# Optimization experiments

Hardware: AMD Instinct MI355X
Metric: run time of the kernel (lower is better)

Reference implementation:

```python
import math
import jax, jax.numpy as jnp
import numpy as np

MUL = 8      # multiplicity of 0e and 1o in irreps_in/out
KS = 5       # kernel spatial extent (diameter 5, steps 1 -> coords -2..2)
NB = 5       # num_radial_basis
RAD = 2.5    # diameter / 2


def _sus(t):
    # e3nn sus(x) = exp(-1/x) for x>0 else 0
    return jnp.where(t > 0.0, jnp.exp(-1.0 / jnp.where(t > 0.0, t, 1.0)), 0.0)


def _emb_sh():
    c = jnp.arange(-2.0, 3.0)
    lat = jnp.stack(jnp.meshgrid(c, c, c, indexing='ij'), axis=-1)  # (5,5,5,3)
    d = jnp.linalg.norm(lat, axis=-1)
    # soft_one_hot_linspace(basis='smooth_finite', cutoff=True)
    values = jnp.linspace(0.0, RAD, NB + 2)
    step = values[1] - values[0]
    diff = (d[..., None] - values[1:-1]) / step
    emb = 1.14136 * math.exp(2.0) * _sus(diff + 1.0) * _sus(1.0 - diff)  # (5,5,5,NB)
    # real spherical harmonics, lmax=2, normalize=True, normalization='component'
    safe = jnp.where(d > 0.0, d, 1.0)[..., None]
    u = jnp.where(d[..., None] > 0.0, lat / safe, 0.0)
    x, y, z = u[..., 0], u[..., 1], u[..., 2]
    s3, s5, s15 = math.sqrt(3.0), math.sqrt(5.0), math.sqrt(15.0)
    sh = jnp.stack([
        jnp.ones_like(x),
        s3 * x, s3 * y, s3 * z,
        s15 * x * z, s15 * x * y,
        s5 * (y * y - 0.5 * (x * x + z * z)),
        s15 * y * z, (s15 / 2.0) * (z * z - x * x),
    ], axis=-1)  # (5,5,5,9)
    return emb, sh


def _c121():
    # Clebsch-Gordan (w3j) for 1o x 2e -> 1o in the real e3nn basis, built from the
    # orthonormal symmetric-traceless matrix basis matching the l=2 SH component order.
    s2, s6 = math.sqrt(2.0), math.sqrt(6.0)
    S = np.zeros((5, 3, 3))
    S[0, 0, 2] = S[0, 2, 0] = 1.0 / s2            # xz
    S[1, 0, 1] = S[1, 1, 0] = 1.0 / s2            # xy
    S[2] = np.diag([-1.0, 2.0, -1.0]) / s6        # 2y^2 - x^2 - z^2
    S[3, 1, 2] = S[3, 2, 1] = 1.0 / s2            # yz
    S[4] = np.diag([-1.0, 0.0, 1.0]) / s2         # z^2 - x^2
    # w3j(1,2,1)[m,j,k] = S[j,m,k]/sqrt(5)  (fully symmetric since l1+l2+l3 even)
    return jnp.asarray(np.transpose(S, (1, 0, 2)) / math.sqrt(5.0), dtype=jnp.float32)


def _build_kernel(weight, emb, sh, c121, dtype):
    g = (KS, KS, KS)
    W = (emb @ weight) / float(KS * KS * KS)  # (5,5,5,320)
    w1, w2, w3, w4, w5 = [W[..., 64 * i:64 * (i + 1)].reshape(g + (MUL, MUL)) for i in range(5)]
    sh0, sh1, sh2 = sh[..., 0], sh[..., 1:4], sh[..., 4:9]
    pw0 = math.sqrt(1.0 / 16.0)   # output 0e: alpha=1, fan_in=8+8
    pw1 = math.sqrt(3.0 / 24.0)   # output 1o: alpha=3, fan_in=8+8+8
    inv_s3 = 1.0 / math.sqrt(3.0)
    K00 = pw0 * sh0[..., None, None] * w1                                   # (g,u,w)
    K01 = (pw1 * inv_s3) * jnp.einsum('xyzuw,xyzk->xyzuwk', w2, sh1)        # (g,u,w,k)
    K10 = (pw0 * inv_s3) * jnp.einsum('xyzuw,xyzm->xyzumw', w4, sh1)        # (g,u,m,w)
    T = jnp.einsum('xyzj,mjk->xyzmk', sh2, c121)                            # (g,m,k)
    eye3 = jnp.eye(3, dtype=dtype)
    K11 = pw1 * (inv_s3 * jnp.einsum('xyzuw,mk->xyzumwk', sh0[..., None, None] * w3, eye3)
                 + jnp.einsum('xyzuw,xyzmk->xyzumwk', w5, T))               # (g,u,m,w,k)
    D = 4 * MUL
    kern = jnp.zeros(g + (D, D), dtype=dtype)
    kern = kern.at[..., :MUL, :MUL].set(K00)
    kern = kern.at[..., :MUL, MUL:].set(K01.reshape(g + (MUL, 3 * MUL)))
    kern = kern.at[..., MUL:, :MUL].set(K10.reshape(g + (3 * MUL, MUL)))
    kern = kern.at[..., MUL:, MUL:].set(K11.reshape(g + (3 * MUL, 3 * MUL)))
    return jnp.transpose(kern, (4, 3, 0, 1, 2))  # 'xyzio->oixyz'


def reference(x, weight, w_sc0, w_sc1):
    emb, sh = _emb_sh()
    c121 = _c121()
    kern = _build_kernel(weight, emb, sh, c121, x.dtype)
    B, _, X, Y, Z = x.shape
    inv_s8 = 1.0 / math.sqrt(MUL)
    # self-connection: e3nn Linear, 0e->0e and 1o->1o blocks
    x0 = x[:, :MUL]
    x1 = x[:, MUL:].reshape(B, MUL, 3, X, Y, Z)
    sc0 = inv_s8 * jnp.einsum('uv,buxyz->bvxyz', w_sc0, x0)
    sc1 = inv_s8 * jnp.einsum('uv,bumxyz->bvmxyz', w_sc1, x1).reshape(B, 3 * MUL, X, Y, Z)
    sc = jnp.concatenate([sc0, sc1], axis=1)
    conv = jax.lax.conv_general_dilated(
        x, kern, window_strides=(1, 1, 1), padding=[(2, 2)] * 3,
        dimension_numbers=('NCDHW', 'OIDHW', 'NCDHW'))
    return sc + conv


def setup_inputs() -> dict:
    key = jax.random.key(0)
    k1, k2, k3, k4 = jax.random.split(key, 4)
    return {
        'x': jax.random.normal(k1, (2, 32, 64, 64, 64), dtype=jnp.float32),
        'weight': jax.random.normal(k2, (NB, 5 * MUL * MUL), dtype=jnp.float32),
        'w_sc0': jax.random.normal(k3, (MUL, MUL), dtype=jnp.float32),
        'w_sc1': jax.random.normal(k4, (MUL, MUL), dtype=jnp.float32),
    }
```

## Files before the change

kernel.cpp:

```cpp
#include <hip/hip_runtime.h>
#include <math.h>

typedef __attribute__((ext_vector_type(8))) short short8;
typedef __attribute__((ext_vector_type(4))) float f32x4;
typedef __attribute__((ext_vector_type(16))) float f32x16;

#define NTAP 125
#define DCH 32

static __device__ __forceinline__ unsigned short f2bf(float f) {
    union { float f; unsigned u; } v; v.f = f;
    unsigned u = v.u;
    return (unsigned short)((u + 0x7FFFu + ((u >> 16) & 1u)) >> 16);
}

static __device__ __forceinline__ void gld_lds16(const void* g, void* l) {
    __builtin_amdgcn_global_load_lds(
        (const __attribute__((address_space(1))) unsigned int*)g,
        (__attribute__((address_space(3))) unsigned int*)l, 16, 0, 0);
}

__global__ __launch_bounds__(128) void build_kern(
    const float* __restrict__ weight,
    const float* __restrict__ w_sc0,
    const float* __restrict__ w_sc1,
    float* __restrict__ kw)
{
    const int t = blockIdx.x;
    const int dx = t / 25, dy = (t / 5) % 5, dz = t % 5;
    const float px = dx - 2.0f, py = dy - 2.0f, pz = dz - 2.0f;
    const float d = sqrtf(px * px + py * py + pz * pz);

    const float stepv = 2.5f / 6.0f;
    const float embc = 1.14136f * expf(2.0f);
    float emb[5];
#pragma unroll
    for (int n = 0; n < 5; ++n) {
        float diff = (d - stepv * (float)(n + 1)) / stepv;
        float a = diff + 1.0f, bb = 1.0f - diff;
        float v = 0.0f;
        if (a > 0.0f && bb > 0.0f)
            v = embc * expf(-1.0f / a) * expf(-1.0f / bb);
        emb[n] = v;
    }

    const float inv_d = (d > 0.0f) ? 1.0f / d : 0.0f;
    const float ux = px * inv_d, uy = py * inv_d, uz = pz * inv_d;
    const float s3 = 1.73205081f, s5 = 2.23606798f, s15 = 3.87298335f;
    float sh[9];
    sh[0] = 1.0f;
    sh[1] = s3 * ux; sh[2] = s3 * uy; sh[3] = s3 * uz;
    sh[4] = s15 * ux * uz;
    sh[5] = s15 * ux * uy;
    sh[6] = s5 * (uy * uy - 0.5f * (ux * ux + uz * uz));
    sh[7] = s15 * uy * uz;
    sh[8] = 0.5f * s15 * (uz * uz - ux * ux);

    const float i_s2 = 0.70710678f, i_s6 = 0.40824829f, i_s5 = 0.44721360f;
    float T[3][3];
    T[0][0] = i_s5 * (-sh[6] * i_s6 - sh[8] * i_s2);
    T[0][1] = i_s5 * (sh[5] * i_s2);
    T[0][2] = i_s5 * (sh[4] * i_s2);
    T[1][0] = T[0][1];
    T[1][1] = i_s5 * (2.0f * sh[6] * i_s6);
    T[1][2] = i_s5 * (sh[7] * i_s2);
    T[2][0] = T[0][2];
    T[2][1] = T[1][2];
    T[2][2] = i_s5 * (-sh[6] * i_s6 + sh[8] * i_s2);

    __shared__ float Wt[320];
    for (int col = threadIdx.x; col < 320; col += 128) {
        float a = 0.0f;
#pragma unroll
        for (int n = 0; n < 5; ++n) a += emb[n] * weight[n * 320 + col];
        Wt[col] = a * (1.0f / 125.0f);
    }
    __syncthreads();

    const float pw0 = 0.25f;
    const float pw1 = 0.35355339f;
    const float inv_s3 = 0.57735027f;
    const float inv_s8 = 0.35355339f;

    for (int idx = threadIdx.x; idx < 1024; idx += 128) {
        const int o = idx >> 5, i = idx & 31;
        float val;
        if (o < 8) {
            if (i < 8) {
                val = pw0 * Wt[i * 8 + o];
            } else {
                const int u = (i - 8) / 3, m = (i - 8) % 3;
                val = pw0 * inv_s3 * Wt[192 + u * 8 + o] * sh[1 + m];
            }
        } else {
            const int v = (o - 8) / 3, k = (o - 8) % 3;
            if (i < 8) {
                val = pw1 * inv_s3 * Wt[64 + i * 8 + v] * sh[1 + k];
            } else {
                const int u = (i - 8) / 3, m = (i - 8) % 3;
                float tv = Wt[256 + u * 8 + v] * T[m][k];
                if (m == k) tv += inv_s3 * Wt[128 + u * 8 + v];
                val = pw1 * tv;
            }
        }
        if (t == 62) {
            if (o < 8 && i < 8) {
                val += inv_s8 * w_sc0[i * 8 + o];
            } else if (o >= 8 && i >= 8) {
                const int u = (i - 8) / 3, m = (i - 8) % 3;
                const int v = (o - 8) / 3, k = (o - 8) % 3;
                if (m == k) val += inv_s8 * w_sc1[u * 8 + v];
            }
        }
        kw[(i * NTAP + t) * DCH + o] = val;
    }
}

__global__ __launch_bounds__(128) void pack_b(
    const float* __restrict__ kw, unsigned short* __restrict__ kwb)
{
    const int t = blockIdx.x;
    const int tid = threadIdx.x;
    const int kh = tid >> 6, l = tid & 63;
    const int co = l & 31;
    const int cib = kh * 16 + (l >> 5) * 8;
    unsigned short v[8];
#pragma unroll
    for (int j = 0; j < 8; ++j)
        v[j] = f2bf(kw[((cib + j) * NTAP + t) * DCH + co]);
    uint4 o;
    o.x = (unsigned)v[0] | ((unsigned)v[1] << 16);
    o.y = (unsigned)v[2] | ((unsigned)v[3] << 16);
    o.z = (unsigned)v[4] | ((unsigned)v[5] << 16);
    o.w = (unsigned)v[6] | ((unsigned)v[7] << 16);
    *reinterpret_cast<uint4*>(kwb + ((size_t)(t * 2 + kh) * 64 + l) * 8) = o;
}

__global__ __launch_bounds__(256) void xpose(
    const float* __restrict__ x, unsigned short* __restrict__ xt)
{
    const int xx = blockIdx.x, yy = blockIdx.y, b = blockIdx.z;
    const int t = threadIdx.x;
    const int z = t & 63, part = t >> 6;
    const float* src = x + ((((size_t)b * 32) * 64 + xx) * 64 + yy) * 64 + z;
    unsigned short v[8];
#pragma unroll
    for (int j = 0; j < 8; ++j)
        v[j] = f2bf(src[(size_t)(part * 8 + j) * 262144]);
    uint4 o;
    o.x = (unsigned)v[0] | ((unsigned)v[1] << 16);
    o.y = (unsigned)v[2] | ((unsigned)v[3] << 16);
    o.z = (unsigned)v[4] | ((unsigned)v[5] << 16);
    o.w = (unsigned)v[6] | ((unsigned)v[7] << 16);
    *reinterpret_cast<uint4*>(
        xt + ((((size_t)b * 64 + xx) * 64 + yy) * 64 + z) * 32 + part * 8) = o;
}

__global__ void zero_fill(float4* p) {
    p[threadIdx.x] = make_float4(0.f, 0.f, 0.f, 0.f);
}

__global__ __launch_bounds__(512, 4) void conv_mfma(
    const unsigned short* __restrict__ xt,
    const unsigned short* __restrict__ kwb,
    const unsigned short* __restrict__ zpage,
    float* __restrict__ out)
{
    extern __shared__ unsigned short smem[];
    char* lds = (char*)smem;

    const int tid = threadIdx.x;
    const int lane = tid & 63;
    const int wv = tid >> 6;
    const int oy = wv >> 1, zh = wv & 1;
    const int x0 = blockIdx.x * 4, y0 = blockIdx.y * 4;
    const int b = blockIdx.z;
    const int l31 = lane & 31, hi = lane >> 5;

    int abase[5][2];
#pragma unroll
    for (int dz = 0; dz < 5; ++dz) {
        const int s = zh * 32 + l31 + dz;
#pragma unroll
        for (int kh = 0; kh < 2; ++kh) {
            const int cph = (kh * 2 + hi) ^ (s & 3);
            abase[dz][kh] = 51200 + ((((oy * 68 + s) << 2) | cph) << 4);
        }
    }
    const int bbase = lane * 16;

    int srow[3]; long long soff[3]; bool szok[3];
#pragma unroll
    for (int p = 0; p < 3; ++p) {
        const int c = tid + p * 512;
        const int row = c / 272;
        const int rem = c - row * 272;
        const int slot = rem >> 2;
        const int clog = (rem & 3) ^ (slot & 3);
        const int z = slot - 2;
        srow[p] = row;
        szok[p] = ((unsigned)z < 64u);
        soff[p] = (long long)row * 2048 + (long long)z * 32 + clog * 8;
    }

    int bsrc[7];
#pragma unroll
    for (int k = 0; k < 7; ++k) {
        const int c = tid + k * 512;
        const int tp = c >> 7, rem = c & 127;
        const int dxx = tp / 5, dzz = tp - dxx * 5;
        bsrc[k] = (dxx * 25 + dzz) * 128 + rem;
    }

    f32x16 acc[4];
#pragma unroll
    for (int ox = 0; ox < 4; ++ox)
#pragma unroll
        for (int e = 0; e < 16; ++e) acc[ox][e] = 0.0f;

    for (int dy = 0; dy < 5; ++dy) {
        const int yyb = y0 + dy - 2;
#pragma unroll
        for (int xl = 0; xl < 8; ++xl) {
            __syncthreads();
            if (xl == 0) {
#pragma unroll
                for (int k = 0; k < 7; ++k) {
                    const int c0 = wv * 64 + k * 512;
                    if (c0 < 3200) {
                        gld_lds16(kwb + ((size_t)(bsrc[k] + dy * 640)) * 8,
                                  lds + c0 * 16);
                    }
                }
            }
            {
                const int xx = x0 + xl - 2;
                const bool xok = ((unsigned)xx < 64u);
                const long long xyb =
                    (long long)(b * 64 + xx) * 131072 + (long long)yyb * 2048;
#pragma unroll
                for (int p = 0; p < 3; ++p) {
                    const int c0 = wv * 64 + p * 512;
                    if (c0 < 1088) {
                        const int yy = yyb + srow[p];
                        const bool ok =
                            xok && ((unsigned)yy < 64u) && szok[p];
                        const unsigned short* src =
                            ok ? (xt + xyb + soff[p]) : zpage;
                        gld_lds16(src, lds + 51200 + c0 * 16);
                    }
                }
            }
            __syncthreads();

#pragma unroll
            for (int dz = 0; dz < 5; ++dz) {
#pragma unroll
                for (int kh = 0; kh < 2; ++kh) {
                    const short8 a =
                        *reinterpret_cast<const short8*>(lds + abase[dz][kh]);
#pragma unroll
                    for (int ox = 0; ox < 4; ++ox) {
                        const int dxv = xl - ox;
                        if (dxv < 0 || dxv > 4) continue;
                        const short8 bf = *reinterpret_cast<const short8*>(
                            lds + bbase + (((dxv * 5 + dz) * 2 + kh) << 10));
                        acc[ox] = __builtin_amdgcn_mfma_f32_32x32x16_bf16(
                            a, bf, acc[ox], 0, 0, 0);
                    }
                }
            }
        }
    }

    const int yy = y0 + oy;
#pragma unroll
    for (int ox = 0; ox < 4; ++ox) {
        float* base = out +
            ((((size_t)b * 32 + l31) * 64 + (x0 + ox)) * 64 + yy) * 64 +
            zh * 32 + hi * 4;
#pragma unroll
        for (int rq = 0; rq < 4; ++rq) {
            f32x4 v = { acc[ox][rq * 4 + 0], acc[ox][rq * 4 + 1],
                        acc[ox][rq * 4 + 2], acc[ox][rq * 4 + 3] };
            *reinterpret_cast<f32x4*>(base + rq * 8) = v;
        }
    }
}

extern "C" void kernel_launch(void* const* d_in, const int* in_sizes, int n_in,
                              void* d_out, int out_size, void* d_ws, size_t ws_size,
                              hipStream_t stream) {
    const float* x      = (const float*)d_in[0];
    const float* weight = (const float*)d_in[1];
    const float* w_sc0  = (const float*)d_in[2];
    const float* w_sc1  = (const float*)d_in[3];
    float* out = (float*)d_out;

    char* ws = (char*)d_ws;
    unsigned short* xt  = (unsigned short*)ws;
    float*          kwp = (float*)(ws + 33554432);
    unsigned short* kwb = (unsigned short*)(ws + 34066432);
    unsigned short* zpg = (unsigned short*)(ws + 34322432);

    (void)hipFuncSetAttribute((const void*)conv_mfma,
                              hipFuncAttributeMaxDynamicSharedMemorySize,
                              68608);

    hipLaunchKernelGGL(build_kern, dim3(NTAP), dim3(128), 0, stream,
                       weight, w_sc0, w_sc1, kwp);
    hipLaunchKernelGGL(pack_b, dim3(NTAP), dim3(128), 0, stream, kwp, kwb);
    hipLaunchKernelGGL(xpose, dim3(64, 64, 2), dim3(256), 0, stream, x, xt);
    hipLaunchKernelGGL(zero_fill, dim3(1), dim3(256), 0, stream, (float4*)zpg);
    hipLaunchKernelGGL(conv_mfma, dim3(16, 16, 2), dim3(512), 68608, stream,
                       xt, kwb, zpg, out);
}
```

Baseline: 161.1 us.

## Halve conv block to 4 waves, each computing two output rows

The conv kernel now runs 256 threads (4 waves) per block instead of 512. Each wave computes two y output rows, so every B-fragment LDS read feeds two MFMAs and the per-MFMA LDS traffic for B drops. The LDS swizzle changes from (s&3) to ((s>>1)&3), presumably to avoid bank conflicts between the two A reads 4352 bytes apart. In exchange, accumulator registers double (128 floats per lane) and there are fewer waves per block to hide latency, which could limit occupancy.

```diff
diff --git a/kernel.cpp b/kernel.cpp
--- a/kernel.cpp
+++ b/kernel.cpp
@@ -160,7 +160,7 @@
     p[threadIdx.x] = make_float4(0.f, 0.f, 0.f, 0.f);
 }
 
-__global__ __launch_bounds__(512, 4) void conv_mfma(
+__global__ __launch_bounds__(256, 2) void conv_mfma(
     const unsigned short* __restrict__ xt,
     const unsigned short* __restrict__ kwb,
     const unsigned short* __restrict__ zpage,
@@ -172,7 +172,7 @@
     const int tid = threadIdx.x;
     const int lane = tid & 63;
     const int wv = tid >> 6;
-    const int oy = wv >> 1, zh = wv & 1;
+    const int oyp = wv >> 1, zh = wv & 1;
     const int x0 = blockIdx.x * 4, y0 = blockIdx.y * 4;
     const int b = blockIdx.z;
     const int l31 = lane & 31, hi = lane >> 5;
@@ -183,40 +183,42 @@
         const int s = zh * 32 + l31 + dz;
 #pragma unroll
         for (int kh = 0; kh < 2; ++kh) {
-            const int cph = (kh * 2 + hi) ^ (s & 3);
-            abase[dz][kh] = 51200 + ((((oy * 68 + s) << 2) | cph) << 4);
+            const int cph = (kh * 2 + hi) ^ ((s >> 1) & 3);
+            abase[dz][kh] = 51200 + (((((oyp * 2) * 68 + s) << 2) | cph) << 4);
         }
     }
     const int bbase = lane * 16;
 
-    int srow[3]; long long soff[3]; bool szok[3];
-#pragma unroll
-    for (int p = 0; p < 3; ++p) {
-        const int c = tid + p * 512;
+    int srow[5]; int soff[5]; bool szok[5];
+#pragma unroll
+    for (int p = 0; p < 5; ++p) {
+        const int c = tid + p * 256;
         const int row = c / 272;
         const int rem = c - row * 272;
         const int slot = rem >> 2;
-        const int clog = (rem & 3) ^ (slot & 3);
+        const int clog = (rem & 3) ^ ((slot >> 1) & 3);
         const int z = slot - 2;
         srow[p] = row;
         szok[p] = ((unsigned)z < 64u);
-        soff[p] = (long long)row * 2048 + (long long)z * 32 + clog * 8;
-    }
-
-    int bsrc[7];
-#pragma unroll
-    for (int k = 0; k < 7; ++k) {
-        const int c = tid + k * 512;
+        soff[p] = row * 2048 + z * 32 + clog * 8;
+    }
+
+    int bsrc[13];
+#pragma unroll
+    for (int k = 0; k < 13; ++k) {
+        const int c = tid + k * 256;
         const int tp = c >> 7, rem = c & 127;
         const int dxx = tp / 5, dzz = tp - dxx * 5;
         bsrc[k] = (dxx * 25 + dzz) * 128 + rem;
     }
 
-    f32x16 acc[4];
-#pragma unroll
-    for (int ox = 0; ox < 4; ++ox)
-#pragma unroll
-        for (int e = 0; e < 16; ++e) acc[ox][e] = 0.0f;
+    f32x16 acc[2][4];
+#pragma unroll
+    for (int oyi = 0; oyi < 2; ++oyi)
+#pragma unroll
+        for (int ox = 0; ox < 4; ++ox)
+#pragma unroll
+            for (int e = 0; e < 16; ++e) acc[oyi][ox][e] = 0.0f;
 
     for (int dy = 0; dy < 5; ++dy) {
         const int yyb = y0 + dy - 2;
@@ -225,8 +227,8 @@
             __syncthreads();
             if (xl == 0) {
 #pragma unroll
-                for (int k = 0; k < 7; ++k) {
-                    const int c0 = wv * 64 + k * 512;
+                for (int k = 0; k < 13; ++k) {
+                    const int c0 = wv * 64 + k * 256;
                     if (c0 < 3200) {
                         gld_lds16(kwb + ((size_t)(bsrc[k] + dy * 640)) * 8,
                                   lds + c0 * 16);
@@ -239,8 +241,8 @@
                 const long long xyb =
                     (long long)(b * 64 + xx) * 131072 + (long long)yyb * 2048;
 #pragma unroll
-                for (int p = 0; p < 3; ++p) {
-                    const int c0 = wv * 64 + p * 512;
+                for (int p = 0; p < 5; ++p) {
+                    const int c0 = wv * 64 + p * 256;
                     if (c0 < 1088) {
                         const int yy = yyb + srow[p];
                         const bool ok =
@@ -257,33 +259,40 @@
             for (int dz = 0; dz < 5; ++dz) {
 #pragma unroll
                 for (int kh = 0; kh < 2; ++kh) {
-                    const short8 a =
+                    const short8 a0 =
                         *reinterpret_cast<const short8*>(lds + abase[dz][kh]);
+                    const short8 a1 = *reinterpret_cast<const short8*>(
+                        lds + abase[dz][kh] + 4352);
 #pragma unroll
                     for (int ox = 0; ox < 4; ++ox) {
                         const int dxv = xl - ox;
                         if (dxv < 0 || dxv > 4) continue;
                         const short8 bf = *reinterpret_cast<const short8*>(
                             lds + bbase + (((dxv * 5 + dz) * 2 + kh) << 10));
-                        acc[ox] = __builtin_amdgcn_mfma_f32_32x32x16_bf16(
-                            a, bf, acc[ox], 0, 0, 0);
+                        acc[0][ox] = __builtin_amdgcn_mfma_f32_32x32x16_bf16(
+                            a0, bf, acc[0][ox], 0, 0, 0);
+                        acc[1][ox] = __builtin_amdgcn_mfma_f32_32x32x16_bf16(
+                            a1, bf, acc[1][ox], 0, 0, 0);
                     }
                 }
             }
         }
     }
 
-    const int yy = y0 + oy;
-#pragma unroll
-    for (int ox = 0; ox < 4; ++ox) {
-        float* base = out +
-            ((((size_t)b * 32 + l31) * 64 + (x0 + ox)) * 64 + yy) * 64 +
-            zh * 32 + hi * 4;
-#pragma unroll
-        for (int rq = 0; rq < 4; ++rq) {
-            f32x4 v = { acc[ox][rq * 4 + 0], acc[ox][rq * 4 + 1],
-                        acc[ox][rq * 4 + 2], acc[ox][rq * 4 + 3] };
-            *reinterpret_cast<f32x4*>(base + rq * 8) = v;
+#pragma unroll
+    for (int oyi = 0; oyi < 2; ++oyi) {
+        const int yy = y0 + oyp * 2 + oyi;
+#pragma unroll
+        for (int ox = 0; ox < 4; ++ox) {
+            float* base = out +
+                ((((size_t)b * 32 + l31) * 64 + (x0 + ox)) * 64 + yy) * 64 +
+                zh * 32 + hi * 4;
+#pragma unroll
+            for (int rq = 0; rq < 4; ++rq) {
+                f32x4 v = { acc[oyi][ox][rq * 4 + 0], acc[oyi][ox][rq * 4 + 1],
+                            acc[oyi][ox][rq * 4 + 2], acc[oyi][ox][rq * 4 + 3] };
+                *reinterpret_cast<f32x4*>(base + rq * 8) = v;
+            }
         }
     }
 }
@@ -312,6 +321,6 @@
     hipLaunchKernelGGL(pack_b, dim3(NTAP), dim3(128), 0, stream, kwp, kwb);
     hipLaunchKernelGGL(xpose, dim3(64, 64, 2), dim3(256), 0, stream, x, xt);
     hipLaunchKernelGGL(zero_fill, dim3(1), dim3(256), 0, stream, (float4*)zpg);
-    hipLaunchKernelGGL(conv_mfma, dim3(16, 16, 2), dim3(512), 68608, stream,
+    hipLaunchKernelGGL(conv_mfma, dim3(16, 16, 2), dim3(256), 68608, stream,
                        xt, kwb, zpg, out);
 }
```

Result: faster. 152.9 us (-5.1%).
